# Kernel optimization log

Hardware: AMD Instinct MI355X
Metric: run time of the kernel (lower is better)

The kernel has to match this reference:

```python
import jax, jax.numpy as jnp
import numpy as np

H = 128            # hardcoded image side in the torch module
TOL = 1e-3         # forward() default tol
MAX_DEPTH = 8      # init kwarg (reduced from 200 for bounded runtime)
LRELU = 0.1        # LeakyReLU negative slope


def _conv(x, w, b, pad):
    # x: [B,Cin,H,H], w: [Cout,Cin,kh,kw]
    y = jax.lax.conv_general_dilated(
        x, w, (1, 1), [(pad, pad), (pad, pad)],
        dimension_numbers=('NCHW', 'OIHW', 'NCHW'))
    if b is not None:
        y = y + b[None, :, None, None]
    return y


def _leaky(x):
    return jnp.where(x >= 0, x, LRELU * x)


def _build_apply_T(d, A, w1, b1, w2, b2, w3, b3, wK, delta, alpha, lambd, beta):
    B = d.shape[0]
    Kc = wK.shape[0]
    dcol = d.reshape(B, -1).T                      # [m, B]
    # ConvTranspose2d(K->1, k=3, pad=1) with weight := convK.weight is the
    # adjoint of convK: regular conv with spatially flipped, channel-swapped kernel.
    wKt = jnp.transpose(jnp.flip(wK, (2, 3)), (1, 0, 2, 3))  # [1,K,3,3]

    def K_op(xk):                                  # [N,B] -> [K*N,B]
        x4 = xk.T.reshape(B, 1, H, H)
        return _conv(x4, wK, None, 1).reshape(B, -1).T

    def Kt_op(pk):                                 # [K*N,B] -> [N,B]
        p4 = pk.T.reshape(B, Kc, H, H)
        return _conv(p4, wKt, None, 1).reshape(B, -1).T

    def R_op(pk):                                  # learned residual denoiser
        p = pk.T.reshape(B, Kc, H, H)
        p = p + _leaky(_conv(p, w1, b1, 2))
        p = p + _leaky(_conv(p, w2, b2, 2))
        p = p + _leaky(_conv(p, w3, b3, 2))
        return p.reshape(B, -1).T

    def ball_proj(w):                              # eval-mode projection
        de = jnp.exp(delta)                        # (1,) -> broadcasts over batch
        dist = jnp.maximum(jnp.linalg.norm(w - dcol, axis=0), 1e-10)
        dn = jnp.linalg.norm(dcol, axis=0)
        scale = jnp.minimum(jnp.ones_like(dist), de * dn / dist)
        return dcol + scale * (w - dcol)

    a = jnp.clip(alpha, 0.0, 2.0)
    bta = jnp.clip(beta, 0.0, 2.0)
    lam = jnp.clip(lambd, 0.0, 2.0)

    def apply_T(x):                                # x: [B,1,H,H]
        xk = x.reshape(B, -1).T                    # [N,B]
        Kxk = K_op(xk)
        # torch: pk = K(xk); pk += lambd*(nuk1 + alpha*(K(xk)-pk)) with nuk1=0
        # and pk==K(xk), so the update is identity -> pk = Kxk.
        pk = R_op(Kxk)
        Axk = A @ xk                               # [m,B]
        # torch: wk = A@xk; temp = wk + lambd*(nuk2 + alpha*(Axk-wk)) = Axk.
        wk = ball_proj(Axk)
        nuk1p = a * (Kxk - pk)
        nuk2p = a * (Axk - wk)
        # nuk1 = nuk2 = 0, so 2*nuk_plus - nuk = 2*nuk_plus
        rk = Kt_op(2.0 * nuk1p) + A.T @ (2.0 * nuk2p)
        xk_new = jnp.clip(xk - bta * rk, 0.0, 1.0)
        return xk_new.T.reshape(B, 1, H, H)

    return apply_T


def setup_inputs() -> dict:
    key = jax.random.key(0)
    ks = jax.random.split(key, 10)
    B, M, N_side, Kc = 8, 4096, 128, 2
    d = jax.random.normal(ks[0], (B, M), jnp.float32)
    A = jax.random.normal(ks[1], (M, N_side * N_side), jnp.float32) / 128.0
    w1 = jax.random.normal(ks[2], (Kc, Kc, 5, 5), jnp.float32) * 0.05
    w2 = jax.random.normal(ks[3], (Kc, Kc, 5, 5), jnp.float32) * 0.05
    w3 = jax.random.normal(ks[4], (Kc, Kc, 5, 5), jnp.float32) * 0.05
    b1 = jnp.zeros((Kc,), jnp.float32)
    b2 = jnp.zeros((Kc,), jnp.float32)
    b3 = jnp.zeros((Kc,), jnp.float32)
    wK = jax.random.normal(ks[5], (Kc, 1, 3, 3), jnp.float32) * 0.1
    return {
        'd': d, 'A': A,
        'w1': w1, 'b1': b1, 'w2': w2, 'b2': b2, 'w3': w3, 'b3': b3,
        'wK': wK,
        'delta': jnp.full((1,), -5.0, jnp.float32),
        'alpha': jnp.full((1,), 0.1, jnp.float32),
        'lambd': jnp.full((1,), 0.1, jnp.float32),
        'beta': jnp.full((1,), 0.1, jnp.float32),
    }


def reference(d, A, w1, b1, w2, b2, w3, b3, wK, delta, alpha, lambd, beta):
    B = d.shape[0]
    apply_T = _build_apply_T(d, A, w1, b1, w2, b2, w3, b3, wK,
                             delta, alpha, lambd, beta)
    x0 = jnp.zeros((B, 1, H, H), d.dtype)
    xp0 = jnp.full((B, 1, H, H), jnp.inf, d.dtype)

    def cond(state):
        x, xp, k = state
        res = jnp.max(jnp.linalg.norm((x - xp).reshape(B, -1), axis=1))
        return (res > TOL) & (k < MAX_DEPTH)

    def body(state):
        x, xp, k = state
        return (apply_T(x), x, k + 1)

    x_star, _, _ = jax.lax.while_loop(cond, body, (x0, xp0, jnp.int32(0)))
    # final differentiable application T(x*)
    return apply_T(x_star)
```

## Files before the change

kernel.cpp:

```cpp
#include <hip/hip_runtime.h>
#include <math.h>

#define HH 128
#define NPIX 16384
#define BB 8
#define MM 4096
#define NN 16384
#define KC 2
#define LRELU_S 0.1f

__device__ __forceinline__ float leaky_(float v){ return v >= 0.f ? v : LRELU_S*v; }
__device__ __forceinline__ float clamp01(float v){ return fminf(fmaxf(v, 0.f), 1.f); }
__device__ __forceinline__ float clamp02(float v){ return fminf(fmaxf(v, 0.f), 2.f); }

__global__ __launch_bounds__(256) void k_convK(const float* __restrict__ x,
                                               const float* __restrict__ wK,
                                               float* __restrict__ out){
  int idx = blockIdx.x*256 + threadIdx.x;
  if (idx >= BB*KC*NPIX) return;
  int j = idx & 127, i = (idx>>7) & 127, c = (idx>>14) & 1, b = idx>>15;
  const float* xb = x + b*NPIX;
  float s = 0.f;
  #pragma unroll
  for (int di=0; di<3; ++di){
    int ii = i + di - 1;
    if ((unsigned)ii >= 128u) continue;
    #pragma unroll
    for (int dj=0; dj<3; ++dj){
      int jj = j + dj - 1;
      if ((unsigned)jj >= 128u) continue;
      s += xb[ii*HH + jj] * wK[(c*3+di)*3 + dj];
    }
  }
  out[idx] = s;
}

__global__ __launch_bounds__(256) void k_conv5(const float* __restrict__ in,
                                               const float* __restrict__ w,
                                               const float* __restrict__ bias,
                                               float* __restrict__ out,
                                               const float* __restrict__ Kx,
                                               const float* __restrict__ alpha,
                                               int fuse_nu){
  int idx = blockIdx.x*256 + threadIdx.x;
  if (idx >= BB*KC*NPIX) return;
  int j = idx & 127, i = (idx>>7) & 127, o = (idx>>14) & 1, b = idx>>15;
  const float* inb = in + b*KC*NPIX;
  float s = bias[o];
  #pragma unroll
  for (int c=0; c<KC; ++c){
    const float* pc = inb + c*NPIX;
    const float* wc = w + (o*KC + c)*25;
    #pragma unroll
    for (int di=0; di<5; ++di){
      int ii = i + di - 2;
      if ((unsigned)ii >= 128u) continue;
      #pragma unroll
      for (int dj=0; dj<5; ++dj){
        int jj = j + dj - 2;
        if ((unsigned)jj >= 128u) continue;
        s += pc[ii*HH + jj] * wc[di*5 + dj];
      }
    }
  }
  float p = in[idx] + leaky_(s);
  if (fuse_nu){
    float a = clamp02(alpha[0]);
    out[idx] = 2.f*a*(Kx[idx] - p);
  } else {
    out[idx] = p;
  }
}

__global__ __launch_bounds__(256) void k_convKt(const float* __restrict__ nu,
                                                const float* __restrict__ wK,
                                                float* __restrict__ rk){
  int idx = blockIdx.x*256 + threadIdx.x;
  if (idx >= BB*NPIX) return;
  int j = idx & 127, i = (idx>>7) & 127, b = idx>>14;
  float s = 0.f;
  #pragma unroll
  for (int c=0; c<KC; ++c){
    const float* pc = nu + (b*KC + c)*NPIX;
    #pragma unroll
    for (int di=0; di<3; ++di){
      int ii = i + di - 1;
      if ((unsigned)ii >= 128u) continue;
      #pragma unroll
      for (int dj=0; dj<3; ++dj){
        int jj = j + dj - 1;
        if ((unsigned)jj >= 128u) continue;
        s += pc[ii*HH + jj] * wK[(c*3 + (2-di))*3 + (2-dj)];
      }
    }
  }
  rk[idx] = s;
}

__global__ __launch_bounds__(256) void k_dn(const float* __restrict__ d, float* __restrict__ dn){
  int b = blockIdx.x, t = threadIdx.x;
  float ss = 0.f;
  for (int m=t; m<MM; m+=256){ float v = d[b*MM + m]; ss += v*v; }
  #pragma unroll
  for (int off=32; off; off>>=1) ss += __shfl_down(ss, off);
  __shared__ float red[4];
  if ((t & 63) == 0) red[t>>6] = ss;
  __syncthreads();
  if (t == 0) dn[b] = sqrtf(red[0]+red[1]+red[2]+red[3]);
}

#define G1_TM 32
#define G1_NT 1024
#define G1_NS (NN/G1_NT)
__global__ __launch_bounds__(256) void k_gemm1(const float* __restrict__ A_,
                                               const float* __restrict__ x,
                                               float* __restrict__ y){
  __shared__ float xs[BB][G1_NT];
  int blk = blockIdx.x;
  int mblk = blk / G1_NS, nblk = blk % G1_NS;
  int m0 = mblk*G1_TM, n0 = nblk*G1_NT;
  int t = threadIdx.x;
  for (int i=t; i < BB*G1_NT/4; i += 256){
    int b = i >> 8;
    int j4 = i & 255;
    *(float4*)&xs[b][j4*4] = *(const float4*)&x[(size_t)b*NN + n0 + j4*4];
  }
  __syncthreads();
  int r = t >> 3, c = t & 7;
  float acc[BB] = {0.f,0.f,0.f,0.f,0.f,0.f,0.f,0.f};
  const float* Ar = A_ + (size_t)(m0 + r)*NN + n0 + c*4;
  #pragma unroll 4
  for (int k=0; k<G1_NT/32; ++k){
    float4 a4 = *(const float4*)(Ar + k*32);
    #pragma unroll
    for (int b=0; b<BB; ++b){
      const float* xp = &xs[b][c*4 + k*32];
      acc[b] += a4.x*xp[0] + a4.y*xp[1] + a4.z*xp[2] + a4.w*xp[3];
    }
  }
  #pragma unroll
  for (int mask=1; mask<8; mask<<=1)
    #pragma unroll
    for (int b=0; b<BB; ++b) acc[b] += __shfl_xor(acc[b], mask);
  if (c == 0){
    #pragma unroll
    for (int b=0; b<BB; ++b) atomicAdd(&y[b*MM + m0 + r], acc[b]);
  }
}

__global__ __launch_bounds__(256) void k_proj(const float* __restrict__ y,
                                              const float* __restrict__ d,
                                              const float* __restrict__ dn,
                                              const float* __restrict__ delta,
                                              const float* __restrict__ alpha,
                                              float* __restrict__ z){
  int b = blockIdx.x, t = threadIdx.x;
  float ss = 0.f;
  for (int m=t; m<MM; m+=256){
    float r = y[b*MM + m] - d[b*MM + m];
    z[b*MM + m] = r;
    ss += r*r;
  }
  #pragma unroll
  for (int off=32; off; off>>=1) ss += __shfl_down(ss, off);
  __shared__ float red[4];
  if ((t & 63) == 0) red[t>>6] = ss;
  __syncthreads();
  float dist = fmaxf(sqrtf(red[0]+red[1]+red[2]+red[3]), 1e-10f);
  float de = expf(delta[0]);
  float a  = clamp02(alpha[0]);
  float scale = fminf(1.f, de*dn[b]/dist);
  float coef = 2.f*a*(1.f - scale);
  for (int m=t; m<MM; m+=256) z[b*MM + m] *= coef;
}

#define G2_MS 32
#define G2_MT (MM/G2_MS)
#define G2_NB 16
#define G2_NT (NN/G2_NB)
__global__ __launch_bounds__(256) void k_gemm2(const float* __restrict__ A_,
                                               const float* __restrict__ z,
                                               float* __restrict__ up){
  __shared__ float zs[BB][G2_MT];
  int blk = blockIdx.x;
  int ms = blk / G2_NB, nb = blk % G2_NB;
  int mbase = ms*G2_MT, n0 = nb*G2_NT;
  int t = threadIdx.x;
  for (int i=t; i < BB*G2_MT; i += 256){
    int b = i >> 7, ml = i & 127;
    zs[b][ml] = z[b*MM + mbase + ml];
  }
  __syncthreads();
  float4 acc[BB];
  #pragma unroll
  for (int b=0; b<BB; ++b){ acc[b].x=0.f; acc[b].y=0.f; acc[b].z=0.f; acc[b].w=0.f; }
  const float* Ac = A_ + (size_t)mbase*NN + n0 + t*4;
  for (int ml=0; ml<G2_MT; ++ml){
    float4 a4 = *(const float4*)(Ac + (size_t)ml*NN);
    #pragma unroll
    for (int b=0; b<BB; ++b){
      float s = zs[b][ml];
      acc[b].x += a4.x*s; acc[b].y += a4.y*s; acc[b].z += a4.z*s; acc[b].w += a4.w*s;
    }
  }
  #pragma unroll
  for (int b=0; b<BB; ++b)
    *(float4*)&up[((size_t)ms*BB + b)*NN + n0 + t*4] = acc[b];
}

__global__ __launch_bounds__(256) void k_combine(float* __restrict__ x,
                                                 const float* __restrict__ rk,
                                                 const float* __restrict__ up,
                                                 const float* __restrict__ beta){
  int idx = blockIdx.x*256 + threadIdx.x;
  if (idx >= BB*NN/4) return;
  float bta = clamp02(beta[0]);
  float4 acc = *(const float4*)&rk[idx*4];
  #pragma unroll 8
  for (int ms=0; ms<G2_MS; ++ms){
    float4 u4 = *(const float4*)&up[(size_t)ms*BB*NN + idx*4];
    acc.x += u4.x; acc.y += u4.y; acc.z += u4.z; acc.w += u4.w;
  }
  float4 xv = *(const float4*)&x[idx*4];
  xv.x = clamp01(xv.x - bta*acc.x);
  xv.y = clamp01(xv.y - bta*acc.y);
  xv.z = clamp01(xv.z - bta*acc.z);
  xv.w = clamp01(xv.w - bta*acc.w);
  *(float4*)&x[idx*4] = xv;
}

extern "C" void kernel_launch(void* const* d_in, const int* in_sizes, int n_in,
                              void* d_out, int out_size, void* d_ws, size_t ws_size,
                              hipStream_t stream) {
  const float* d_d   = (const float*)d_in[0];
  const float* d_A   = (const float*)d_in[1];
  const float* w1    = (const float*)d_in[2];
  const float* b1    = (const float*)d_in[3];
  const float* w2    = (const float*)d_in[4];
  const float* b2    = (const float*)d_in[5];
  const float* w3    = (const float*)d_in[6];
  const float* b3    = (const float*)d_in[7];
  const float* wK    = (const float*)d_in[8];
  const float* delta = (const float*)d_in[9];
  const float* alpha = (const float*)d_in[10];
  const float* beta  = (const float*)d_in[12];

  float* ws = (float*)d_ws;
  size_t off = 0;
  float* x   = ws + off; off += (size_t)BB*NN;
  float* Kx  = ws + off; off += (size_t)BB*KC*NPIX;
  float* t1  = ws + off; off += (size_t)BB*KC*NPIX;
  float* t2  = ws + off; off += (size_t)BB*KC*NPIX;
  float* rk1 = ws + off; off += (size_t)BB*NN;
  float* y   = ws + off; off += (size_t)BB*MM;
  float* z   = ws + off; off += (size_t)BB*MM;
  float* dnb = ws + off; off += 8;
  float* up  = ws + off; off += (size_t)G2_MS*BB*NN;

  hipMemsetAsync(x, 0, (size_t)BB*NN*sizeof(float), stream);
  k_dn<<<BB, 256, 0, stream>>>(d_d, dnb);

  for (int it=0; it<9; ++it){
    k_convK <<<1024, 256, 0, stream>>>(x, wK, Kx);
    k_conv5 <<<1024, 256, 0, stream>>>(Kx, w1, b1, t1, nullptr, nullptr, 0);
    k_conv5 <<<1024, 256, 0, stream>>>(t1, w2, b2, t2, nullptr, nullptr, 0);
    k_conv5 <<<1024, 256, 0, stream>>>(t2, w3, b3, t1, Kx, alpha, 1);
    k_convKt<<< 512, 256, 0, stream>>>(t1, wK, rk1);

    hipMemsetAsync(y, 0, (size_t)BB*MM*sizeof(float), stream);
    k_gemm1 <<<(MM/G1_TM)*G1_NS, 256, 0, stream>>>(d_A, x, y);
    k_proj  <<<BB, 256, 0, stream>>>(y, d_d, dnb, delta, alpha, z);
    k_gemm2 <<<G2_MS*G2_NB, 256, 0, stream>>>(d_A, z, up);
    k_combine<<<(BB*NN/4+255)/256, 256, 0, stream>>>(x, rk1, up, beta);
  }

  hipMemcpyAsync(d_out, x, (size_t)BB*NN*sizeof(float), hipMemcpyDeviceToDevice, stream);
}
```

Baseline: 1.480 ms.

## Fuse conv chain into one kernel and run A-products as bf16 MFMA

Replaces the five separate conv kernels with a single row-slab kernel that keeps all intermediates in shared memory with halos. Converts A once per call to bf16 in both row-major and transposed packed layouts, and computes both A·x and Aᵀ·z with 16x16x32 bf16 MFMA instructions instead of fp32 FMA loops. The projection and combine kernels are restructured to match. This halves the bytes of A streamed per iteration and cuts launches, but adds a full conversion pass over A on every call and bf16 rounding error in the data-consistency terms.

```diff
diff --git a/kernel.cpp b/kernel.cpp
--- a/kernel.cpp
+++ b/kernel.cpp
@@ -9,92 +9,43 @@
 #define KC 2
 #define LRELU_S 0.1f
 
+typedef __attribute__((ext_vector_type(8))) short bf16x8;
+typedef __attribute__((ext_vector_type(4))) float f32x4;
+
 __device__ __forceinline__ float leaky_(float v){ return v >= 0.f ? v : LRELU_S*v; }
 __device__ __forceinline__ float clamp01(float v){ return fminf(fmaxf(v, 0.f), 1.f); }
 __device__ __forceinline__ float clamp02(float v){ return fminf(fmaxf(v, 0.f), 2.f); }
-
-__global__ __launch_bounds__(256) void k_convK(const float* __restrict__ x,
-                                               const float* __restrict__ wK,
-                                               float* __restrict__ out){
-  int idx = blockIdx.x*256 + threadIdx.x;
-  if (idx >= BB*KC*NPIX) return;
-  int j = idx & 127, i = (idx>>7) & 127, c = (idx>>14) & 1, b = idx>>15;
-  const float* xb = x + b*NPIX;
-  float s = 0.f;
-  #pragma unroll
-  for (int di=0; di<3; ++di){
-    int ii = i + di - 1;
-    if ((unsigned)ii >= 128u) continue;
-    #pragma unroll
-    for (int dj=0; dj<3; ++dj){
-      int jj = j + dj - 1;
-      if ((unsigned)jj >= 128u) continue;
-      s += xb[ii*HH + jj] * wK[(c*3+di)*3 + dj];
-    }
-  }
-  out[idx] = s;
-}
-
-__global__ __launch_bounds__(256) void k_conv5(const float* __restrict__ in,
-                                               const float* __restrict__ w,
-                                               const float* __restrict__ bias,
-                                               float* __restrict__ out,
-                                               const float* __restrict__ Kx,
-                                               const float* __restrict__ alpha,
-                                               int fuse_nu){
-  int idx = blockIdx.x*256 + threadIdx.x;
-  if (idx >= BB*KC*NPIX) return;
-  int j = idx & 127, i = (idx>>7) & 127, o = (idx>>14) & 1, b = idx>>15;
-  const float* inb = in + b*KC*NPIX;
-  float s = bias[o];
-  #pragma unroll
-  for (int c=0; c<KC; ++c){
-    const float* pc = inb + c*NPIX;
-    const float* wc = w + (o*KC + c)*25;
-    #pragma unroll
-    for (int di=0; di<5; ++di){
-      int ii = i + di - 2;
-      if ((unsigned)ii >= 128u) continue;
-      #pragma unroll
-      for (int dj=0; dj<5; ++dj){
-        int jj = j + dj - 2;
-        if ((unsigned)jj >= 128u) continue;
-        s += pc[ii*HH + jj] * wc[di*5 + dj];
-      }
-    }
-  }
-  float p = in[idx] + leaky_(s);
-  if (fuse_nu){
-    float a = clamp02(alpha[0]);
-    out[idx] = 2.f*a*(Kx[idx] - p);
-  } else {
-    out[idx] = p;
-  }
-}
-
-__global__ __launch_bounds__(256) void k_convKt(const float* __restrict__ nu,
-                                                const float* __restrict__ wK,
-                                                float* __restrict__ rk){
-  int idx = blockIdx.x*256 + threadIdx.x;
-  if (idx >= BB*NPIX) return;
-  int j = idx & 127, i = (idx>>7) & 127, b = idx>>14;
-  float s = 0.f;
-  #pragma unroll
-  for (int c=0; c<KC; ++c){
-    const float* pc = nu + (b*KC + c)*NPIX;
-    #pragma unroll
-    for (int di=0; di<3; ++di){
-      int ii = i + di - 1;
-      if ((unsigned)ii >= 128u) continue;
-      #pragma unroll
-      for (int dj=0; dj<3; ++dj){
-        int jj = j + dj - 1;
-        if ((unsigned)jj >= 128u) continue;
-        s += pc[ii*HH + jj] * wK[(c*3 + (2-di))*3 + (2-dj)];
-      }
-    }
-  }
-  rk[idx] = s;
+__device__ __forceinline__ unsigned short f2bf(float f){
+  unsigned u = __float_as_uint(f);
+  u = (u + 0x7FFFu + ((u >> 16) & 1u)) >> 16;
+  return (unsigned short)u;
+}
+
+__global__ __launch_bounds__(256) void k_prep(const float* __restrict__ A_,
+                                              unsigned short* __restrict__ Abf,
+                                              unsigned short* __restrict__ Atp){
+  __shared__ float lds[64][65];
+  int bm = blockIdx.x >> 8, bn = blockIdx.x & 255;
+  int m0 = bm*64, n0 = bn*64;
+  int t = threadIdx.x;
+  for (int i=t; i<64*16; i+=256){
+    int r = i >> 4, c4 = i & 15;
+    float4 v = *(const float4*)&A_[(size_t)(m0+r)*NN + n0 + c4*4];
+    lds[r][c4*4+0]=v.x; lds[r][c4*4+1]=v.y; lds[r][c4*4+2]=v.z; lds[r][c4*4+3]=v.w;
+  }
+  __syncthreads();
+  for (int i=t; i<64*16; i+=256){
+    int r = i >> 4, c4 = i & 15;
+    unsigned short o[4];
+    for (int j=0;j<4;++j) o[j] = f2bf(lds[r][c4*4+j]);
+    *(uint2*)&Abf[(size_t)(m0+r)*NN + n0 + c4*4] = *(uint2*)o;
+  }
+  for (int i=t; i<8*64; i+=256){
+    int mbl = i >> 6, nl = i & 63;
+    unsigned short o[8];
+    for (int j=0;j<8;++j) o[j] = f2bf(lds[mbl*8+j][nl]);
+    *(uint4*)&Atp[((size_t)(m0/8 + mbl)*NN + n0 + nl)*8] = *(uint4*)o;
+  }
 }
 
 __global__ __launch_bounds__(256) void k_dn(const float* __restrict__ d, float* __restrict__ dn){
@@ -109,124 +60,257 @@
   if (t == 0) dn[b] = sqrtf(red[0]+red[1]+red[2]+red[3]);
 }
 
-#define G1_TM 32
-#define G1_NT 1024
-#define G1_NS (NN/G1_NT)
-__global__ __launch_bounds__(256) void k_gemm1(const float* __restrict__ A_,
-                                               const float* __restrict__ x,
-                                               float* __restrict__ y){
-  __shared__ float xs[BB][G1_NT];
+__global__ __launch_bounds__(256) void k_conv_chain(const float* __restrict__ x,
+    const float* __restrict__ wK, const float* __restrict__ w1, const float* __restrict__ b1,
+    const float* __restrict__ w2, const float* __restrict__ b2,
+    const float* __restrict__ w3, const float* __restrict__ b3,
+    const float* __restrict__ alpha, float* __restrict__ rk){
+  __shared__ float xs[24][128];
+  __shared__ float bufA[2][22][128];
+  __shared__ float bufB[2][18][128];
+  __shared__ float wKs[18], w1s[100], w2s[100], w3s[100], bs[3][2];
+  __shared__ float twoa;
   int blk = blockIdx.x;
-  int mblk = blk / G1_NS, nblk = blk % G1_NS;
-  int m0 = mblk*G1_TM, n0 = nblk*G1_NT;
+  int b = blk >> 4, slab = blk & 15, r0 = slab*8;
   int t = threadIdx.x;
-  for (int i=t; i < BB*G1_NT/4; i += 256){
-    int b = i >> 8;
-    int j4 = i & 255;
-    *(float4*)&xs[b][j4*4] = *(const float4*)&x[(size_t)b*NN + n0 + j4*4];
-  }
-  __syncthreads();
-  int r = t >> 3, c = t & 7;
-  float acc[BB] = {0.f,0.f,0.f,0.f,0.f,0.f,0.f,0.f};
-  const float* Ar = A_ + (size_t)(m0 + r)*NN + n0 + c*4;
-  #pragma unroll 4
-  for (int k=0; k<G1_NT/32; ++k){
-    float4 a4 = *(const float4*)(Ar + k*32);
-    #pragma unroll
-    for (int b=0; b<BB; ++b){
-      const float* xp = &xs[b][c*4 + k*32];
-      acc[b] += a4.x*xp[0] + a4.y*xp[1] + a4.z*xp[2] + a4.w*xp[3];
-    }
-  }
-  #pragma unroll
-  for (int mask=1; mask<8; mask<<=1)
-    #pragma unroll
-    for (int b=0; b<BB; ++b) acc[b] += __shfl_xor(acc[b], mask);
-  if (c == 0){
-    #pragma unroll
-    for (int b=0; b<BB; ++b) atomicAdd(&y[b*MM + m0 + r], acc[b]);
-  }
-}
-
-__global__ __launch_bounds__(256) void k_proj(const float* __restrict__ y,
-                                              const float* __restrict__ d,
-                                              const float* __restrict__ dn,
-                                              const float* __restrict__ delta,
-                                              const float* __restrict__ alpha,
-                                              float* __restrict__ z){
-  int b = blockIdx.x, t = threadIdx.x;
-  float ss = 0.f;
-  for (int m=t; m<MM; m+=256){
-    float r = y[b*MM + m] - d[b*MM + m];
-    z[b*MM + m] = r;
-    ss += r*r;
-  }
-  #pragma unroll
-  for (int off=32; off; off>>=1) ss += __shfl_down(ss, off);
-  __shared__ float red[4];
-  if ((t & 63) == 0) red[t>>6] = ss;
-  __syncthreads();
-  float dist = fmaxf(sqrtf(red[0]+red[1]+red[2]+red[3]), 1e-10f);
-  float de = expf(delta[0]);
-  float a  = clamp02(alpha[0]);
-  float scale = fminf(1.f, de*dn[b]/dist);
-  float coef = 2.f*a*(1.f - scale);
-  for (int m=t; m<MM; m+=256) z[b*MM + m] *= coef;
-}
-
-#define G2_MS 32
-#define G2_MT (MM/G2_MS)
-#define G2_NB 16
-#define G2_NT (NN/G2_NB)
-__global__ __launch_bounds__(256) void k_gemm2(const float* __restrict__ A_,
-                                               const float* __restrict__ z,
-                                               float* __restrict__ up){
-  __shared__ float zs[BB][G2_MT];
+  for (int i=t;i<18;i+=256) wKs[i]=wK[i];
+  for (int i=t;i<100;i+=256){ w1s[i]=w1[i]; w2s[i]=w2[i]; w3s[i]=w3[i]; }
+  if (t<2){ bs[0][t]=b1[t]; bs[1][t]=b2[t]; bs[2][t]=b3[t]; }
+  if (t==0) twoa = 2.f*clamp02(alpha[0]);
+  for (int idx=t; idx<24*128; idx+=256){
+    int i = idx>>7, j = idx&127, ir = r0-8+i;
+    xs[i][j] = ((unsigned)ir < 128u) ? x[b*NPIX + ir*HH + j] : 0.f;
+  }
+  __syncthreads();
+  for (int c=0;c<2;++c)
+    for (int idx=t; idx<22*128; idx+=256){
+      int i = idx>>7, j = idx&127, ir = r0-7+i;
+      float s = 0.f;
+      if ((unsigned)ir < 128u){
+        #pragma unroll
+        for (int di=0;di<3;++di){
+          #pragma unroll
+          for (int dj=0;dj<3;++dj){
+            int jj = j+dj-1;
+            if ((unsigned)jj < 128u) s += xs[i+di][jj]*wKs[(c*3+di)*3+dj];
+          }
+        }
+      }
+      bufA[c][i][j] = s;
+    }
+  __syncthreads();
+  for (int o=0;o<2;++o)
+    for (int idx=t; idx<18*128; idx+=256){
+      int i = idx>>7, j = idx&127, ir = r0-5+i;
+      float v = 0.f;
+      if ((unsigned)ir < 128u){
+        float s = bs[0][o];
+        #pragma unroll
+        for (int c=0;c<2;++c)
+          #pragma unroll
+          for (int di=0;di<5;++di)
+            #pragma unroll
+            for (int dj=0;dj<5;++dj){
+              int jj = j+dj-2;
+              if ((unsigned)jj < 128u) s += bufA[c][i+di][jj]*w1s[(o*2+c)*25+di*5+dj];
+            }
+        v = bufA[o][i+2][j] + leaky_(s);
+      }
+      bufB[o][i][j] = v;
+    }
+  __syncthreads();
+  for (int o=0;o<2;++o)
+    for (int idx=t; idx<14*128; idx+=256){
+      int i = idx>>7, j = idx&127, ir = r0-3+i;
+      float v = 0.f;
+      if ((unsigned)ir < 128u){
+        float s = bs[1][o];
+        #pragma unroll
+        for (int c=0;c<2;++c)
+          #pragma unroll
+          for (int di=0;di<5;++di)
+            #pragma unroll
+            for (int dj=0;dj<5;++dj){
+              int jj = j+dj-2;
+              if ((unsigned)jj < 128u) s += bufB[c][i+di][jj]*w2s[(o*2+c)*25+di*5+dj];
+            }
+        v = bufB[o][i+2][j] + leaky_(s);
+      }
+      bufA[o][i][j] = v;
+    }
+  __syncthreads();
+  for (int o=0;o<2;++o)
+    for (int idx=t; idx<10*128; idx+=256){
+      int i = idx>>7, j = idx&127, ir = r0-1+i;
+      float v = 0.f;
+      if ((unsigned)ir < 128u){
+        float s = bs[2][o];
+        #pragma unroll
+        for (int c=0;c<2;++c)
+          #pragma unroll
+          for (int di=0;di<5;++di)
+            #pragma unroll
+            for (int dj=0;dj<5;++dj){
+              int jj = j+dj-2;
+              if ((unsigned)jj < 128u) s += bufA[c][i+di][jj]*w3s[(o*2+c)*25+di*5+dj];
+            }
+        v = bufA[o][i+2][j] + leaky_(s);
+      }
+      bufB[o][i][j] = v;
+    }
+  __syncthreads();
+  for (int c=0;c<2;++c)
+    for (int idx=t; idx<10*128; idx+=256){
+      int i = idx>>7, j = idx&127, ir = r0-1+i;
+      float v = 0.f;
+      if ((unsigned)ir < 128u){
+        float kx = 0.f;
+        #pragma unroll
+        for (int di=0;di<3;++di)
+          #pragma unroll
+          for (int dj=0;dj<3;++dj){
+            int jj = j+dj-1;
+            if ((unsigned)jj < 128u) kx += xs[i+6+di][jj]*wKs[(c*3+di)*3+dj];
+          }
+        v = twoa*(kx - bufB[c][i][j]);
+      }
+      bufA[c][i][j] = v;
+    }
+  __syncthreads();
+  for (int idx=t; idx<8*128; idx+=256){
+    int i = idx>>7, j = idx&127, ir = r0+i;
+    float s = 0.f;
+    #pragma unroll
+    for (int c=0;c<2;++c)
+      #pragma unroll
+      for (int di=0;di<3;++di)
+        #pragma unroll
+        for (int dj=0;dj<3;++dj){
+          int jj = j+dj-1;
+          if ((unsigned)jj < 128u) s += bufA[c][i+di][jj]*wKs[(c*3+(2-di))*3+(2-dj)];
+        }
+    rk[b*NPIX + ir*HH + j] = s;
+  }
+}
+
+__global__ __launch_bounds__(512) void k_gemm1mf(const unsigned short* __restrict__ Abf,
+    const unsigned short* __restrict__ xtt, const float* __restrict__ d_,
+    float* __restrict__ e_, float* __restrict__ d2p){
+  int mt = blockIdx.x;
+  int w = threadIdx.x >> 6;
+  int lane = threadIdx.x & 63;
+  int kg = lane >> 4, col = lane & 15;
+  const unsigned short* Ap = Abf + (size_t)(mt*16 + col)*NN + w*2048 + kg*8;
+  const unsigned short* Bp = xtt + ((size_t)(w*256 + kg)*16 + col)*8;
+  f32x4 acc = {0.f,0.f,0.f,0.f};
+  #pragma unroll 8
+  for (int s=0; s<64; ++s){
+    bf16x8 a = *(const bf16x8*)(Ap + s*32);
+    bf16x8 b = *(const bf16x8*)(Bp + s*512);
+    acc = __builtin_amdgcn_mfma_f32_16x16x32_bf16(a, b, acc, 0, 0, 0);
+  }
+  __shared__ float part[8][16][16];
+  __shared__ float p2[16][16];
+  #pragma unroll
+  for (int j=0;j<4;++j) part[w][kg*4+j][col] = acc[j];
+  __syncthreads();
+  int t = threadIdx.x;
+  if (t < 256){
+    int r = t >> 4, b = t & 15;
+    float s = 0.f;
+    #pragma unroll
+    for (int w2=0; w2<8; ++w2) s += part[w2][r][b];
+    int m = mt*16 + r;
+    float ee = s - ((b < 8) ? d_[b*MM + m] : 0.f);
+    e_[m*16 + b] = ee;
+    p2[r][b] = (b < 8) ? ee*ee : 0.f;
+  }
+  __syncthreads();
+  if (t < 8){
+    float s2 = 0.f;
+    #pragma unroll
+    for (int r2=0;r2<16;++r2) s2 += p2[r2][t];
+    d2p[mt*8 + t] = s2;
+  }
+}
+
+__global__ __launch_bounds__(256) void k_zt(const float* __restrict__ e_,
+    const float* __restrict__ d2p, const float* __restrict__ dn,
+    const float* __restrict__ delta, const float* __restrict__ alpha,
+    unsigned short* __restrict__ zt){
+  __shared__ float red[32][8];
+  __shared__ float cf[8];
+  int t = threadIdx.x;
+  {
+    int b = t & 7, chunk = t >> 3;
+    float s = 0.f;
+    #pragma unroll
+    for (int i=0;i<8;++i) s += d2p[(chunk + 32*i)*8 + b];
+    red[chunk][b] = s;
+  }
+  __syncthreads();
+  if (t < 8){
+    float s2 = 0.f;
+    #pragma unroll
+    for (int c=0;c<32;++c) s2 += red[c][t];
+    float dist = fmaxf(sqrtf(s2), 1e-10f);
+    float de = expf(delta[0]);
+    float a = clamp02(alpha[0]);
+    float scale = fminf(1.f, de*dn[t]/dist);
+    cf[t] = 2.f*a*(1.f - scale);
+  }
+  __syncthreads();
+  int m0 = blockIdx.x*128;
+  for (int idx=t; idx<128*16; idx+=256){
+    int ml = idx >> 4, b = idx & 15, m = m0 + ml;
+    float v = (b < 8) ? cf[b]*e_[m*16 + b] : 0.f;
+    zt[(size_t)(m>>3)*128 + b*8 + (m&7)] = f2bf(v);
+  }
+}
+
+__global__ __launch_bounds__(64) void k_gemm2mf(const unsigned short* __restrict__ Atp,
+    const unsigned short* __restrict__ zt, float* __restrict__ up){
   int blk = blockIdx.x;
-  int ms = blk / G2_NB, nb = blk % G2_NB;
-  int mbase = ms*G2_MT, n0 = nb*G2_NT;
-  int t = threadIdx.x;
-  for (int i=t; i < BB*G2_MT; i += 256){
-    int b = i >> 7, ml = i & 127;
-    zs[b][ml] = z[b*MM + mbase + ml];
-  }
-  __syncthreads();
-  float4 acc[BB];
-  #pragma unroll
-  for (int b=0; b<BB; ++b){ acc[b].x=0.f; acc[b].y=0.f; acc[b].z=0.f; acc[b].w=0.f; }
-  const float* Ac = A_ + (size_t)mbase*NN + n0 + t*4;
-  for (int ml=0; ml<G2_MT; ++ml){
-    float4 a4 = *(const float4*)(Ac + (size_t)ml*NN);
-    #pragma unroll
-    for (int b=0; b<BB; ++b){
-      float s = zs[b][ml];
-      acc[b].x += a4.x*s; acc[b].y += a4.y*s; acc[b].z += a4.z*s; acc[b].w += a4.w*s;
-    }
-  }
-  #pragma unroll
-  for (int b=0; b<BB; ++b)
-    *(float4*)&up[((size_t)ms*BB + b)*NN + n0 + t*4] = acc[b];
-}
-
-__global__ __launch_bounds__(256) void k_combine(float* __restrict__ x,
-                                                 const float* __restrict__ rk,
-                                                 const float* __restrict__ up,
-                                                 const float* __restrict__ beta){
-  int idx = blockIdx.x*256 + threadIdx.x;
-  if (idx >= BB*NN/4) return;
+  int nt = blk >> 1, ms = blk & 1;
+  int lane = threadIdx.x;
+  int kg = lane >> 4, nc = lane & 15;
+  const unsigned short* Ap = zt  + ((size_t)(ms*256 + kg)*16 + nc)*8;
+  const unsigned short* Bp = Atp + ((size_t)(ms*256 + kg)*NN + nt*16 + nc)*8;
+  f32x4 acc = {0.f,0.f,0.f,0.f};
+  #pragma unroll 8
+  for (int s=0; s<64; ++s){
+    bf16x8 a = *(const bf16x8*)(Ap + (size_t)s*512);
+    bf16x8 b = *(const bf16x8*)(Bp + (size_t)s*4*NN*8);
+    acc = __builtin_amdgcn_mfma_f32_16x16x32_bf16(a, b, acc, 0, 0, 0);
+  }
+  #pragma unroll
+  for (int j=0;j<4;++j)
+    up[(size_t)(ms*16 + kg*4 + j)*NN + nt*16 + nc] = acc[j];
+}
+
+__global__ __launch_bounds__(256) void k_combine2(const float* __restrict__ up,
+    const float* __restrict__ rk, const float* __restrict__ beta,
+    float* __restrict__ x, unsigned short* __restrict__ xtt){
+  int gid = blockIdx.x*256 + threadIdx.x;
+  int b = gid >> 11, nb = gid & 2047, n0 = nb*8;
+  if (b >= 8){
+    uint4 z = {0,0,0,0};
+    *(uint4*)&xtt[(size_t)(nb*16 + b)*8] = z;
+    return;
+  }
   float bta = clamp02(beta[0]);
-  float4 acc = *(const float4*)&rk[idx*4];
-  #pragma unroll 8
-  for (int ms=0; ms<G2_MS; ++ms){
-    float4 u4 = *(const float4*)&up[(size_t)ms*BB*NN + idx*4];
-    acc.x += u4.x; acc.y += u4.y; acc.z += u4.z; acc.w += u4.w;
-  }
-  float4 xv = *(const float4*)&x[idx*4];
-  xv.x = clamp01(xv.x - bta*acc.x);
-  xv.y = clamp01(xv.y - bta*acc.y);
-  xv.z = clamp01(xv.z - bta*acc.z);
-  xv.w = clamp01(xv.w - bta*acc.w);
-  *(float4*)&x[idx*4] = xv;
+  float xv[8]; unsigned short o[8];
+  #pragma unroll
+  for (int j=0;j<8;++j){
+    float v = rk[b*NPIX + n0 + j]
+            + up[(size_t)(0*16 + b)*NN + n0 + j]
+            + up[(size_t)(1*16 + b)*NN + n0 + j];
+    xv[j] = clamp01(x[b*NPIX + n0 + j] - bta*v);
+    o[j] = f2bf(xv[j]);
+  }
+  #pragma unroll
+  for (int j=0;j<8;++j) x[b*NPIX + n0 + j] = xv[j];
+  *(uint4*)&xtt[(size_t)(nb*16 + b)*8] = *(uint4*)o;
 }
 
 extern "C" void kernel_launch(void* const* d_in, const int* in_sizes, int n_in,
@@ -245,34 +329,30 @@
   const float* alpha = (const float*)d_in[10];
   const float* beta  = (const float*)d_in[12];
 
-  float* ws = (float*)d_ws;
-  size_t off = 0;
-  float* x   = ws + off; off += (size_t)BB*NN;
-  float* Kx  = ws + off; off += (size_t)BB*KC*NPIX;
-  float* t1  = ws + off; off += (size_t)BB*KC*NPIX;
-  float* t2  = ws + off; off += (size_t)BB*KC*NPIX;
-  float* rk1 = ws + off; off += (size_t)BB*NN;
-  float* y   = ws + off; off += (size_t)BB*MM;
-  float* z   = ws + off; off += (size_t)BB*MM;
-  float* dnb = ws + off; off += 8;
-  float* up  = ws + off; off += (size_t)G2_MS*BB*NN;
-
-  hipMemsetAsync(x, 0, (size_t)BB*NN*sizeof(float), stream);
+  char* p = (char*)d_ws;
+  unsigned short* Abf = (unsigned short*)p; p += (size_t)MM*NN*2;
+  unsigned short* Atp = (unsigned short*)p; p += (size_t)MM*NN*2;
+  unsigned short* xtt = (unsigned short*)p; p += (size_t)2048*16*8*2;
+  unsigned short* zt  = (unsigned short*)p; p += (size_t)512*16*8*2;
+  float* x   = (float*)p; p += (size_t)BB*NPIX*4;
+  float* rk1 = (float*)p; p += (size_t)BB*NPIX*4;
+  float* e_  = (float*)p; p += (size_t)MM*16*4;
+  float* up  = (float*)p; p += (size_t)2*16*NN*4;
+  float* d2p = (float*)p; p += (size_t)256*8*4;
+  float* dnb = (float*)p; p += 64;
+
+  k_prep<<<64*256, 256, 0, stream>>>(d_A, Abf, Atp);
   k_dn<<<BB, 256, 0, stream>>>(d_d, dnb);
+  hipMemsetAsync(x, 0, (size_t)BB*NPIX*4, stream);
+  hipMemsetAsync(xtt, 0, (size_t)2048*16*8*2, stream);
 
   for (int it=0; it<9; ++it){
-    k_convK <<<1024, 256, 0, stream>>>(x, wK, Kx);
-    k_conv5 <<<1024, 256, 0, stream>>>(Kx, w1, b1, t1, nullptr, nullptr, 0);
-    k_conv5 <<<1024, 256, 0, stream>>>(t1, w2, b2, t2, nullptr, nullptr, 0);
-    k_conv5 <<<1024, 256, 0, stream>>>(t2, w3, b3, t1, Kx, alpha, 1);
-    k_convKt<<< 512, 256, 0, stream>>>(t1, wK, rk1);
-
-    hipMemsetAsync(y, 0, (size_t)BB*MM*sizeof(float), stream);
-    k_gemm1 <<<(MM/G1_TM)*G1_NS, 256, 0, stream>>>(d_A, x, y);
-    k_proj  <<<BB, 256, 0, stream>>>(y, d_d, dnb, delta, alpha, z);
-    k_gemm2 <<<G2_MS*G2_NB, 256, 0, stream>>>(d_A, z, up);
-    k_combine<<<(BB*NN/4+255)/256, 256, 0, stream>>>(x, rk1, up, beta);
-  }
-
-  hipMemcpyAsync(d_out, x, (size_t)BB*NN*sizeof(float), hipMemcpyDeviceToDevice, stream);
-}
+    k_conv_chain<<<128, 256, 0, stream>>>(x, wK, w1, b1, w2, b2, w3, b3, alpha, rk1);
+    k_gemm1mf<<<256, 512, 0, stream>>>(Abf, xtt, d_d, e_, d2p);
+    k_zt<<<32, 256, 0, stream>>>(e_, d2p, dnb, delta, alpha, zt);
+    k_gemm2mf<<<2048, 64, 0, stream>>>(Atp, zt, up);
+    k_combine2<<<128, 256, 0, stream>>>(up, rk1, beta, x, xtt);
+  }
+
+  hipMemcpyAsync(d_out, x, (size_t)BB*NPIX*4, hipMemcpyDeviceToDevice, stream);
+}
```

Result: no change. 1.467 ms (-0.9%).
